# Optimization experiments

Measured on AMD Instinct MI355X. Metric: run time of the kernel, lower is better.

The kernel has to match this reference:

```python
import jax, jax.numpy as jnp
import numpy as np

B, S, DIM = 2, 2048, 4096
N_HEADS, N_KV_HEADS = 32, 8
HEAD_DIM = DIM // N_HEADS  # 128
N_REP = N_HEADS // N_KV_HEADS  # 4
NEG_INF = -1e9


def setup_inputs() -> dict:
    key = jax.random.key(0)
    ks = jax.random.split(key, 6)
    x = jax.random.normal(ks[0], (B, S, DIM), dtype=jnp.float32)
    # torch Linear weights are [out_features, in_features]
    sc = 0.02
    wq = jax.random.normal(ks[1], (N_HEADS * HEAD_DIM, DIM), dtype=jnp.float32) * sc
    wk = jax.random.normal(ks[2], (N_KV_HEADS * HEAD_DIM, DIM), dtype=jnp.float32) * sc
    wv = jax.random.normal(ks[3], (N_KV_HEADS * HEAD_DIM, DIM), dtype=jnp.float32) * sc
    wo = jax.random.normal(ks[4], (DIM, N_HEADS * HEAD_DIM), dtype=jnp.float32) * sc
    # RoPE frequencies, matching llama precompute_freqs_cis (theta=10000)
    inv = 1.0 / (10000.0 ** (np.arange(0, HEAD_DIM, 2, dtype=np.float32) / HEAD_DIM))
    t = np.arange(S, dtype=np.float32)
    freqs = np.outer(t, inv)  # [S, HEAD_DIM//2]
    freqs_cos = jnp.asarray(np.cos(freqs), dtype=jnp.float32)
    freqs_sin = jnp.asarray(np.sin(freqs), dtype=jnp.float32)
    # causal mask: 0 on/below diagonal, large negative above
    mask = jnp.triu(jnp.full((S, S), NEG_INF, dtype=jnp.float32), k=1)
    return {"x": x, "wq": wq, "wk": wk, "wv": wv, "wo": wo,
            "freqs_cos": freqs_cos, "freqs_sin": freqs_sin,
            "mask": mask, "start_pos": 0}


def _apply_rope(t, cos, sin):
    # t: [b, s, h, hd]; complex mult on interleaved (even, odd) pairs
    tr, ti = t[..., 0::2], t[..., 1::2]
    cos = cos[None, :, None, :]
    sin = sin[None, :, None, :]
    out_r = tr * cos - ti * sin
    out_i = tr * sin + ti * cos
    return jnp.stack([out_r, out_i], axis=-1).reshape(t.shape)


def reference(x, wq, wk, wv, wo, freqs_cos, freqs_sin, mask, start_pos):
    bsz, seqlen, _ = x.shape
    xq = (x @ wq.T).reshape(bsz, seqlen, N_HEADS, HEAD_DIM)
    xk = (x @ wk.T).reshape(bsz, seqlen, N_KV_HEADS, HEAD_DIM)
    xv = (x @ wv.T).reshape(bsz, seqlen, N_KV_HEADS, HEAD_DIM)
    xq = _apply_rope(xq, freqs_cos, freqs_sin)
    xk = _apply_rope(xk, freqs_cos, freqs_sin)
    # prefill: start_pos == 0, so cache slice == current keys/values
    # GQA repeat_kv via broadcast (torch repeat_interleave over head dim)
    keys = jnp.broadcast_to(xk[:, :, :, None, :],
                            (bsz, seqlen, N_KV_HEADS, N_REP, HEAD_DIM)
                            ).reshape(bsz, seqlen, N_HEADS, HEAD_DIM)
    values = jnp.broadcast_to(xv[:, :, :, None, :],
                              (bsz, seqlen, N_KV_HEADS, N_REP, HEAD_DIM)
                              ).reshape(bsz, seqlen, N_HEADS, HEAD_DIM)
    scale = 1.0 / jnp.sqrt(jnp.float32(HEAD_DIM))
    # [b, h, q, k]
    scores = jnp.einsum('bqhd,bkhd->bhqk', xq, keys) * scale
    scores = scores + mask[None, None, :, :]
    probs = jax.nn.softmax(scores.astype(jnp.float32), axis=-1).astype(xq.dtype)
    out = jnp.einsum('bhqk,bkhd->bqhd', probs, values)
    out = out.reshape(bsz, seqlen, N_HEADS * HEAD_DIM)
    return out @ wo.T
```

## Files before the change

### kernel.cpp

```cpp
#include <hip/hip_runtime.h>

typedef unsigned short u16;
typedef unsigned int u32;
typedef __bf16 bf16_t;
typedef bf16_t bf16x8 __attribute__((ext_vector_type(8)));
typedef float f32x4 __attribute__((ext_vector_type(4)));

#define B_ 2
#define S_ 2048
#define DIM_ 4096
#define NH_ 32
#define NKV_ 8
#define HD_ 128

__device__ __forceinline__ u16 f2b(float f) {
  union { float f; unsigned u; } x; x.f = f;
  unsigned r = x.u + 0x7fffu + ((x.u >> 16) & 1u);
  return (u16)(r >> 16);
}
__device__ __forceinline__ float b2f(u16 u) {
  union { unsigned u; float f; } x; x.u = ((unsigned)u) << 16;
  return x.f;
}
__device__ __forceinline__ u32 cvtpk(float lo, float hi) {
  u32 r;
  asm volatile("v_cvt_pk_bf16_f32 %0, %1, %2" : "=v"(r) : "v"(lo), "v"(hi));
  return r;
}

#define GLDS(gsrc, ldst) \
  __builtin_amdgcn_global_load_lds((const __attribute__((address_space(1))) void*)(gsrc), \
                                   (__attribute__((address_space(3))) void*)(ldst), 16, 0, 0)
#define BAR()    __builtin_amdgcn_s_barrier()
#define SCHED0() __builtin_amdgcn_sched_barrier(0)

__global__ void cvt_kernel(const float* __restrict__ in, u16* __restrict__ out, int n4) {
  int i = blockIdx.x * blockDim.x + threadIdx.x;
  int stride = gridDim.x * blockDim.x;
  for (; i < n4; i += stride) {
    float4 v = ((const float4*)in)[i];
    ushort4 o;
    o.x = f2b(v.x); o.y = f2b(v.y); o.z = f2b(v.z); o.w = f2b(v.w);
    ((ushort4*)out)[i] = o;
  }
}

__global__ void rope_kernel(u16* __restrict__ t, const float* __restrict__ fc,
                            const float* __restrict__ fs, int nheads) {
  int idx = blockIdx.x * blockDim.x + threadIdx.x;
  int ppr = nheads * 64;
  int row = idx / ppr;
  int pr = idx - row * ppr;
  int h = pr >> 6, j = pr & 63;
  int s = row & (S_ - 1);
  float c = fc[s * 64 + j], sn = fs[s * 64 + j];
  u16* p = t + (size_t)row * (size_t)(nheads * HD_) + h * HD_ + j * 2;
  float tr = b2f(p[0]), ti = b2f(p[1]);
  p[0] = f2b(tr * c - ti * sn);
  p[1] = f2b(tr * sn + ti * c);
}

template<int MODE>
__global__ __launch_bounds__(512, 2) void gemm256(const u16* __restrict__ A,
                                                  const u16* __restrict__ B,
                                                  void* __restrict__ Cout,
                                                  void* __restrict__ Cout2,
                                                  void* __restrict__ Cout3,
                                                  int M, int N, int K) {
  __shared__ u16 As[2][2][128 * 64];
  __shared__ u16 Bs[2][2][128 * 64];
  const int nbn = N >> 8;
  const int nwg = gridDim.x;
  int wg = blockIdx.x;
  wg = (wg & 7) * (nwg >> 3) + (wg >> 3);
  const int bm = wg / nbn;
  const int bn = wg - bm * nbn;
  const int tid = threadIdx.x;
  const int lane = tid & 63;
  const int wv = tid >> 6;
  const int wm = wv >> 2, wn = wv & 3;
  const int qloc = lane & 15, grp = lane >> 4;
  const int NT = K >> 6;

  f32x4 acc[8][4];
#pragma unroll
  for (int i = 0; i < 8; i++)
#pragma unroll
    for (int j = 0; j < 4; j++)
#pragma unroll
      for (int r = 0; r < 4; r++) acc[i][j][r] = 0.0f;

  const int srowl = lane >> 3;
  const int scsw = 8 * ((lane & 7) ^ srowl);
  const size_t rowA = (size_t)(bm * 256 + wv * 16 + srowl) * K + scsw;
  const size_t rowB = (size_t)(bn * 256 + wv * 16 + srowl) * K + scsw;

#define STAGE_A(buf, h, tt) { \
    GLDS(A + rowA + (size_t)((h) * 128) * K + (size_t)(tt) * 64, &As[buf][h][wv * 1024]); \
    GLDS(A + rowA + (size_t)((h) * 128 + 8) * K + (size_t)(tt) * 64, &As[buf][h][wv * 1024 + 512]); }
#define STAGE_B(buf, h, tt) { \
    GLDS(B + rowB + (size_t)((h) * 128) * K + (size_t)(tt) * 64, &Bs[buf][h][wv * 1024]); \
    GLDS(B + rowB + (size_t)((h) * 128 + 8) * K + (size_t)(tt) * 64, &Bs[buf][h][wv * 1024 + 512]); }

  STAGE_A(0, 0, 0); STAGE_A(0, 1, 0);
  STAGE_B(0, 0, 0); STAGE_B(0, 1, 0);
  STAGE_B(1, 0, 1); STAGE_B(1, 1, 1);
  asm volatile("s_waitcnt vmcnt(4)" ::: "memory");
  BAR();

  for (int t = 0; t < NT; t += 2) {
#pragma unroll
    for (int half = 0; half < 2; half++) {
      bf16x8 bfr[4][2];
#pragma unroll
      for (int qd = 0; qd < 4; qd++) {
        if (qd == 0) {
#pragma unroll
          for (int j = 0; j < 4; j++)
#pragma unroll
            for (int ks = 0; ks < 2; ks++) {
              int rb = (wn & 1) * 64 + j * 16 + qloc;
              bfr[j][ks] = *(const bf16x8*)((const char*)&Bs[half][wn >> 1][0]
                           + rb * 128 + ((ks * 64 + grp * 16) ^ ((rb & 7) << 4)));
            }
        }
        bf16x8 af[2][2];
#pragma unroll
        for (int ii = 0; ii < 2; ii++)
#pragma unroll
          for (int ks = 0; ks < 2; ks++) {
            int rh = qd * 32 + ii * 16 + qloc;
            af[ii][ks] = *(const bf16x8*)((const char*)&As[half][wm][0]
                         + rh * 128 + ((ks * 64 + grp * 16) ^ ((rh & 7) << 4)));
          }
        const int ph = half * 4 + qd;
        if (ph == 0)      { STAGE_A(1, 0, t + 1); }
        else if (ph == 1) { STAGE_A(1, 1, t + 1); }
        else if (ph == 2) { if (t + 2 < NT) STAGE_B(0, 0, t + 2); }
        else if (ph == 3) { if (t + 2 < NT) STAGE_B(0, 1, t + 2); }
        else if (ph == 4) { if (t + 2 < NT) STAGE_A(0, 0, t + 2); }
        else if (ph == 5) { if (t + 2 < NT) STAGE_A(0, 1, t + 2); }
        else if (ph == 6) { if (t + 3 < NT) STAGE_B(1, 0, t + 3); }
        else              { if (t + 3 < NT) STAGE_B(1, 1, t + 3); }
        BAR();
        __builtin_amdgcn_s_setprio(1);
#pragma unroll
        for (int ii = 0; ii < 2; ii++)
#pragma unroll
          for (int ks = 0; ks < 2; ks++)
#pragma unroll
            for (int j = 0; j < 4; j++)
              acc[qd * 2 + ii][j] = __builtin_amdgcn_mfma_f32_16x16x32_bf16(
                  af[ii][ks], bfr[j][ks], acc[qd * 2 + ii][j], 0, 0, 0);
        __builtin_amdgcn_s_setprio(0);
        SCHED0();
        if (qd == 3) {
          if ((half == 0 ? t + 2 : t + 3) < NT)
            asm volatile("s_waitcnt vmcnt(4)" ::: "memory");
          else
            asm volatile("s_waitcnt vmcnt(0)" ::: "memory");
        }
        BAR();
      }
    }
  }
#undef STAGE_A
#undef STAGE_B

  const int r0g = bm * 256 + wm * 128 + grp * 4;
  const int c0g = bn * 256 + wn * 64 + qloc;
#pragma unroll
  for (int i = 0; i < 8; i++)
#pragma unroll
    for (int j = 0; j < 4; j++)
#pragma unroll
      for (int r = 0; r < 4; r++) {
        int row = r0g + i * 16 + r;
        int col = c0g + j * 16;
        float v = acc[i][j][r];
        if (MODE == 1) ((float*)Cout)[(size_t)row * N + col] = v;
        else {
          if (col < 4096)      ((u16*)Cout)[(size_t)row * 4096 + col] = f2b(v);
          else if (col < 5120) ((u16*)Cout2)[(size_t)row * 1024 + (col - 4096)] = f2b(v);
          else                 ((u16*)Cout3)[(size_t)(col - 5120) * M + row] = f2b(v);
        }
      }
}

__global__ __launch_bounds__(256) void attn_kernel(const u16* __restrict__ Q,
                                                   const u16* __restrict__ Kt,
                                                   const u16* __restrict__ VT,
                                                   u16* __restrict__ O,
                                                   const float* __restrict__ fc,
                                                   const float* __restrict__ fs) {
  __shared__ u16 Ks[2][32 * 128];
  __shared__ u16 Vs[2][32 * 128];

  const int bid = blockIdx.x;
  const int qb = 31 - (bid >> 6);
  const int h = bid & 31;
  const int b = (bid >> 5) & 1;
  const int g = h >> 2;
  const int tid = threadIdx.x;
  const int lane = tid & 63;
  const int wv = tid >> 6;
  const int qrow0 = qb * 64 + wv * 16;
  const float scl2 = 0.12751744f;

  const int qloc = lane & 15;
  const int grp = lane >> 4;

  bf16x8 qf[4];
  {
    const int qr = qrow0 + qloc;
    const u16* qptr = Q + (size_t)(b * S_ + qr) * (NH_ * HD_) + h * HD_ + grp * 8;
#pragma unroll
    for (int c = 0; c < 4; c++) {
      union { bf16x8 v; u16 u[8]; } raw;
      raw.v = *(const bf16x8*)(qptr + c * 32);
      const int p0 = c * 16 + grp * 4;
      const float4 cv = *(const float4*)&fc[(size_t)qr * 64 + p0];
      const float4 sv = *(const float4*)&fs[(size_t)qr * 64 + p0];
      union { bf16x8 v; u32 w[4]; } out;
      const float cc[4] = {cv.x, cv.y, cv.z, cv.w};
      const float ss[4] = {sv.x, sv.y, sv.z, sv.w};
#pragma unroll
      for (int j = 0; j < 4; j++) {
        float tr = b2f(raw.u[2 * j]), ti = b2f(raw.u[2 * j + 1]);
        out.w[j] = cvtpk(tr * cc[j] - ti * ss[j], tr * ss[j] + ti * cc[j]);
      }
      qf[c] = out.v;
    }
  }

  float m = -1e30f, l = 0.f;
  f32x4 o[8];
#pragma unroll
  for (int c = 0; c < 8; c++)
#pragma unroll
    for (int r = 0; r < 4; r++) o[c][r] = 0.f;

  const int nkv = 2 * qb + 2;

  const int kkey_ = wv * 4 + grp;
  const int kcb_ = qloc * 16;
  const int vd_ = wv * 16 + (lane >> 2);
  const int vkb_ = (lane & 3) * 16;

  auto STAGE = [&](int t, int buf) {
#pragma unroll
    for (int p = 0; p < 2; p++) {
      int key = p * 16 + kkey_;
      int cbs = kcb_ ^ ((key & 7) << 4);
      const u16* ksrc = Kt + (size_t)(b * S_ + t * 32 + key) * (NKV_ * HD_) + g * HD_ + (cbs >> 1);
      GLDS(ksrc, &Ks[buf][(p * 4 + wv) * 512]);
      int d = p * 64 + vd_;
      int kbs = vkb_ ^ (((d >> 1) & 3) << 4);
      const u16* vsrc = VT + (size_t)(g * HD_ + d) * (B_ * S_) + b * S_ + t * 32 + (kbs >> 1);
      GLDS(vsrc, &Vs[buf][(p * 4 + wv) * 512]);
    }
  };

  STAGE(0, 0);
  int cur = 0;

  for (int t = 0; t < nkv; t++) {
    const bool pf = (t + 1 < nkv);
    if (pf) {
      STAGE(t + 1, cur ^ 1);
      asm volatile("s_waitcnt vmcnt(4)" ::: "memory");
    } else {
      asm volatile("s_waitcnt vmcnt(0)" ::: "memory");
    }
    BAR();
    SCHED0();

    if (t * 32 <= qrow0 + 15) {
      f32x4 s[2];
      __builtin_amdgcn_s_setprio(1);
#pragma unroll
      for (int n = 0; n < 2; n++) {
        f32x4 sc;
#pragma unroll
        for (int r = 0; r < 4; r++) sc[r] = 0.f;
        int krow = n * 16 + qloc;
#pragma unroll
        for (int c = 0; c < 4; c++) {
          int colb = c * 64 + (grp * 16);
          int addr = krow * 256 + (colb ^ ((krow & 7) << 4));
          bf16x8 kf = *(const bf16x8*)((const char*)Ks[cur] + addr);
          sc = __builtin_amdgcn_mfma_f32_16x16x32_bf16(kf, qf[c], sc, 0, 0, 0);
        }
        s[n] = sc;
      }
      __builtin_amdgcn_s_setprio(0);
      const int q = qrow0 + qloc;
      if (t * 32 + 31 > qrow0) {
#pragma unroll
        for (int n = 0; n < 2; n++)
#pragma unroll
          for (int r = 0; r < 4; r++) {
            int k = t * 32 + n * 16 + grp * 4 + r;
            if (k > q) s[n][r] = -1e9f;
          }
      }
      float pmax = fmaxf(fmaxf(fmaxf(s[0][0], s[0][1]), fmaxf(s[0][2], s[0][3])),
                         fmaxf(fmaxf(s[1][0], s[1][1]), fmaxf(s[1][2], s[1][3])));
      pmax = fmaxf(pmax, __shfl_xor(pmax, 16));
      pmax = fmaxf(pmax, __shfl_xor(pmax, 32));
      if (__any(pmax > m + 64.f)) {
        float mn = fmaxf(m, pmax);
        float alpha = exp2f((m - mn) * scl2);
        m = mn;
        l *= alpha;
        float ar[4];
#pragma unroll
        for (int r = 0; r < 4; r++) ar[r] = __shfl(alpha, grp * 4 + r);
#pragma unroll
        for (int c = 0; c < 8; c++)
#pragma unroll
          for (int r = 0; r < 4; r++) o[c][r] *= ar[r];
      }
      const float msc = m * scl2;
      float p[2][4];
#pragma unroll
      for (int n = 0; n < 2; n++)
#pragma unroll
        for (int r = 0; r < 4; r++)
          p[n][r] = exp2f(fmaf(s[n][r], scl2, -msc));
      float rs = ((p[0][0] + p[0][1]) + (p[0][2] + p[0][3])) +
                 ((p[1][0] + p[1][1]) + (p[1][2] + p[1][3]));
      rs += __shfl_xor(rs, 16);
      rs += __shfl_xor(rs, 32);
      l += rs;
      u32 a0 = cvtpk(p[0][0], p[0][1]);
      u32 a1 = cvtpk(p[0][2], p[0][3]);
      u32 b0 = cvtpk(p[1][0], p[1][1]);
      u32 b1 = cvtpk(p[1][2], p[1][3]);
      asm volatile("v_permlane32_swap_b32 %0, %1" : "+v"(a0), "+v"(b0));
      asm volatile("v_permlane32_swap_b32 %0, %1" : "+v"(a1), "+v"(b1));
      asm volatile("v_permlane16_swap_b32 %0, %1" : "+v"(a0), "+v"(b0));
      asm volatile("v_permlane16_swap_b32 %0, %1" : "+v"(a1), "+v"(b1));
      union { bf16x8 v; u32 w[4]; } pau;
      pau.w[0] = a0; pau.w[1] = a1; pau.w[2] = b0; pau.w[3] = b1;
      bf16x8 pa = pau.v;
      __builtin_amdgcn_s_setprio(1);
#pragma unroll
      for (int c = 0; c < 8; c++) {
        int d = c * 16 + qloc;
        int addr = d * 64 + ((grp * 16) ^ (((d >> 1) & 3) << 4));
        bf16x8 vf = *(const bf16x8*)((const char*)Vs[cur] + addr);
        o[c] = __builtin_amdgcn_mfma_f32_16x16x32_bf16(pa, vf, o[c], 0, 0, 0);
      }
      __builtin_amdgcn_s_setprio(0);
    }
    asm volatile("s_waitcnt lgkmcnt(0)" ::: "memory");
    SCHED0();
    BAR();
    cur ^= 1;
  }

  float lr[4];
#pragma unroll
  for (int r = 0; r < 4; r++) lr[r] = 1.0f / __shfl(l, grp * 4 + r);
#pragma unroll
  for (int c = 0; c < 8; c++)
#pragma unroll
    for (int r = 0; r < 4; r++) {
      int qo = qrow0 + grp * 4 + r;
      float val = o[c][r] * lr[r];
      O[(size_t)(b * S_ + qo) * (NH_ * HD_) + h * HD_ + c * 16 + qloc] = f2b(val);
    }
}

extern "C" void kernel_launch(void* const* d_in, const int* in_sizes, int n_in,
                              void* d_out, int out_size, void* d_ws, size_t ws_size,
                              hipStream_t stream) {
  const float* x  = (const float*)d_in[0];
  const float* wq = (const float*)d_in[1];
  const float* wk = (const float*)d_in[2];
  const float* wv = (const float*)d_in[3];
  const float* wo = (const float*)d_in[4];
  const float* fc = (const float*)d_in[5];
  const float* fs = (const float*)d_in[6];

  char* ws = (char*)d_ws;
  u16* Xb   = (u16*)(ws);
  u16* Wqkv = (u16*)(ws + 33554432);
  u16* Qw   = (u16*)(ws + 83886080);
  u16* Kw   = (u16*)(ws + 117440512);
  u16* Vw   = (u16*)(ws + 125829120);
  u16* Ow   = Xb;
  u16* Wob  = Wqkv;

  auto cvt = [&](const float* in, u16* out, int n) {
    int n4 = n >> 2;
    int blocks = (n4 + 255) / 256; if (blocks > 2048) blocks = 2048;
    cvt_kernel<<<dim3(blocks), dim3(256), 0, stream>>>(in, out, n4);
  };
  cvt(x,  Xb,  B_ * S_ * DIM_);
  cvt(wq, Wqkv, DIM_ * DIM_);
  cvt(wk, Wqkv + (size_t)4096 * 4096, NKV_ * HD_ * DIM_);
  cvt(wv, Wqkv + (size_t)5120 * 4096, NKV_ * HD_ * DIM_);

  gemm256<4><<<dim3(16 * 24), 512, 0, stream>>>(Xb, Wqkv, Qw, Kw, Vw, 4096, 6144, 4096);

  cvt(wo, Wob, DIM_ * DIM_);

  rope_kernel<<<dim3((B_ * S_ * NKV_ * 64) / 256), 256, 0, stream>>>(Kw, fc, fs, NKV_);

  attn_kernel<<<dim3(B_ * NH_ * (S_ / 64)), 256, 0, stream>>>(Qw, Kw, Vw, Ow, fc, fs);

  gemm256<1><<<dim3(16 * 16), 512, 0, stream>>>(Ow, Wob, d_out, nullptr, nullptr, 4096, 4096, 4096);
}
```

Measured before the change: 568.0 us.

## Split fused QKV GEMM into Q GEMM and a 128-row-tile KV GEMM

```diff
diff --git a/kernel.cpp b/kernel.cpp
--- a/kernel.cpp
+++ b/kernel.cpp
@@ -60,15 +60,18 @@
   p[1] = f2b(tr * sn + ti * c);
 }
 
-template<int MODE>
+template<int MODE, bool SM>
 __global__ __launch_bounds__(512, 2) void gemm256(const u16* __restrict__ A,
                                                   const u16* __restrict__ B,
                                                   void* __restrict__ Cout,
                                                   void* __restrict__ Cout2,
-                                                  void* __restrict__ Cout3,
                                                   int M, int N, int K) {
-  __shared__ u16 As[2][2][128 * 64];
-  __shared__ u16 Bs[2][2][128 * 64];
+  constexpr int BM = SM ? 128 : 256;
+  constexpr int AH = SM ? 4096 : 8192;
+  constexpr int II = SM ? 1 : 2;
+  constexpr int NACC = SM ? 4 : 8;
+  __shared__ u16 As[2][2][AH];
+  __shared__ u16 Bs[2][2][8192];
   const int nbn = N >> 8;
   const int nwg = gridDim.x;
   int wg = blockIdx.x;
@@ -82,9 +85,9 @@
   const int qloc = lane & 15, grp = lane >> 4;
   const int NT = K >> 6;
 
-  f32x4 acc[8][4];
-#pragma unroll
-  for (int i = 0; i < 8; i++)
+  f32x4 acc[NACC][4];
+#pragma unroll
+  for (int i = 0; i < NACC; i++)
 #pragma unroll
     for (int j = 0; j < 4; j++)
 #pragma unroll
@@ -92,12 +95,16 @@
 
   const int srowl = lane >> 3;
   const int scsw = 8 * ((lane & 7) ^ srowl);
-  const size_t rowA = (size_t)(bm * 256 + wv * 16 + srowl) * K + scsw;
+  const size_t rowA = SM ? ((size_t)(bm * 128 + wv * 8 + srowl) * K + scsw)
+                         : ((size_t)(bm * 256 + wv * 16 + srowl) * K + scsw);
   const size_t rowB = (size_t)(bn * 256 + wv * 16 + srowl) * K + scsw;
 
 #define STAGE_A(buf, h, tt) { \
-    GLDS(A + rowA + (size_t)((h) * 128) * K + (size_t)(tt) * 64, &As[buf][h][wv * 1024]); \
-    GLDS(A + rowA + (size_t)((h) * 128 + 8) * K + (size_t)(tt) * 64, &As[buf][h][wv * 1024 + 512]); }
+    if (SM) { \
+      GLDS(A + rowA + (size_t)((h) * 64) * K + (size_t)(tt) * 64, &As[buf][h][wv * 512]); \
+    } else { \
+      GLDS(A + rowA + (size_t)((h) * 128) * K + (size_t)(tt) * 64, &As[buf][h][wv * 1024]); \
+      GLDS(A + rowA + (size_t)((h) * 128 + 8) * K + (size_t)(tt) * 64, &As[buf][h][wv * 1024 + 512]); } }
 #define STAGE_B(buf, h, tt) { \
     GLDS(B + rowB + (size_t)((h) * 128) * K + (size_t)(tt) * 64, &Bs[buf][h][wv * 1024]); \
     GLDS(B + rowB + (size_t)((h) * 128 + 8) * K + (size_t)(tt) * 64, &Bs[buf][h][wv * 1024 + 512]); }
@@ -124,12 +131,12 @@
                            + rb * 128 + ((ks * 64 + grp * 16) ^ ((rb & 7) << 4)));
             }
         }
-        bf16x8 af[2][2];
-#pragma unroll
-        for (int ii = 0; ii < 2; ii++)
+        bf16x8 af[II][2];
+#pragma unroll
+        for (int ii = 0; ii < II; ii++)
 #pragma unroll
           for (int ks = 0; ks < 2; ks++) {
-            int rh = qd * 32 + ii * 16 + qloc;
+            int rh = SM ? (qd * 16 + qloc) : (qd * 32 + ii * 16 + qloc);
             af[ii][ks] = *(const bf16x8*)((const char*)&As[half][wm][0]
                          + rh * 128 + ((ks * 64 + grp * 16) ^ ((rh & 7) << 4)));
           }
@@ -145,13 +152,13 @@
         BAR();
         __builtin_amdgcn_s_setprio(1);
 #pragma unroll
-        for (int ii = 0; ii < 2; ii++)
+        for (int ii = 0; ii < II; ii++)
 #pragma unroll
           for (int ks = 0; ks < 2; ks++)
 #pragma unroll
             for (int j = 0; j < 4; j++)
-              acc[qd * 2 + ii][j] = __builtin_amdgcn_mfma_f32_16x16x32_bf16(
-                  af[ii][ks], bfr[j][ks], acc[qd * 2 + ii][j], 0, 0, 0);
+              acc[qd * II + ii][j] = __builtin_amdgcn_mfma_f32_16x16x32_bf16(
+                  af[ii][ks], bfr[j][ks], acc[qd * II + ii][j], 0, 0, 0);
         __builtin_amdgcn_s_setprio(0);
         SCHED0();
         if (qd == 3) {
@@ -167,10 +174,10 @@
 #undef STAGE_A
 #undef STAGE_B
 
-  const int r0g = bm * 256 + wm * 128 + grp * 4;
+  const int r0g = bm * BM + wm * (BM / 2) + grp * 4;
   const int c0g = bn * 256 + wn * 64 + qloc;
 #pragma unroll
-  for (int i = 0; i < 8; i++)
+  for (int i = 0; i < NACC; i++)
 #pragma unroll
     for (int j = 0; j < 4; j++)
 #pragma unroll
@@ -178,11 +185,11 @@
         int row = r0g + i * 16 + r;
         int col = c0g + j * 16;
         float v = acc[i][j][r];
-        if (MODE == 1) ((float*)Cout)[(size_t)row * N + col] = v;
+        if (MODE == 1)      ((float*)Cout)[(size_t)row * N + col] = v;
+        else if (MODE == 0) ((u16*)Cout)[(size_t)row * N + col]  = f2b(v);
         else {
-          if (col < 4096)      ((u16*)Cout)[(size_t)row * 4096 + col] = f2b(v);
-          else if (col < 5120) ((u16*)Cout2)[(size_t)row * 1024 + (col - 4096)] = f2b(v);
-          else                 ((u16*)Cout3)[(size_t)(col - 5120) * M + row] = f2b(v);
+          if (col < 1024) ((u16*)Cout)[(size_t)row * 1024 + col] = f2b(v);
+          else            ((u16*)Cout2)[(size_t)(col - 1024) * M + row] = f2b(v);
         }
       }
 }
@@ -385,13 +392,14 @@
   const float* fs = (const float*)d_in[6];
 
   char* ws = (char*)d_ws;
-  u16* Xb   = (u16*)(ws);
-  u16* Wqkv = (u16*)(ws + 33554432);
-  u16* Qw   = (u16*)(ws + 83886080);
-  u16* Kw   = (u16*)(ws + 117440512);
-  u16* Vw   = (u16*)(ws + 125829120);
-  u16* Ow   = Xb;
-  u16* Wob  = Wqkv;
+  u16* Xb  = (u16*)(ws);
+  u16* Wqb = (u16*)(ws + 33554432);
+  u16* Wkv = (u16*)(ws + 67108864);
+  u16* Qw  = (u16*)(ws + 83886080);
+  u16* Kw  = (u16*)(ws + 117440512);
+  u16* Vw  = (u16*)(ws + 125829120);
+  u16* Ow  = Xb;
+  u16* Wob = Wqb;
 
   auto cvt = [&](const float* in, u16* out, int n) {
     int n4 = n >> 2;
@@ -399,11 +407,12 @@
     cvt_kernel<<<dim3(blocks), dim3(256), 0, stream>>>(in, out, n4);
   };
   cvt(x,  Xb,  B_ * S_ * DIM_);
-  cvt(wq, Wqkv, DIM_ * DIM_);
-  cvt(wk, Wqkv + (size_t)4096 * 4096, NKV_ * HD_ * DIM_);
-  cvt(wv, Wqkv + (size_t)5120 * 4096, NKV_ * HD_ * DIM_);
-
-  gemm256<4><<<dim3(16 * 24), 512, 0, stream>>>(Xb, Wqkv, Qw, Kw, Vw, 4096, 6144, 4096);
+  cvt(wq, Wqb, DIM_ * DIM_);
+  cvt(wk, Wkv, NKV_ * HD_ * DIM_);
+  cvt(wv, Wkv + (size_t)1024 * 4096, NKV_ * HD_ * DIM_);
+
+  gemm256<0, false><<<dim3(16 * 16), 512, 0, stream>>>(Xb, Wqb, Qw, nullptr, 4096, 4096, 4096);
+  gemm256<3, true><<<dim3(32 * 8), 512, 0, stream>>>(Xb, Wkv, Kw, Vw, 4096, 2048, 4096);
 
   cvt(wo, Wob, DIM_ * DIM_);
 
@@ -411,5 +420,5 @@
 
   attn_kernel<<<dim3(B_ * NH_ * (S_ / 64)), 256, 0, stream>>>(Qw, Kw, Vw, Ow, fc, fs);
 
-  gemm256<1><<<dim3(16 * 16), 512, 0, stream>>>(Ow, Wob, d_out, nullptr, nullptr, 4096, 4096, 4096);
-}
+  gemm256<1, false><<<dim3(16 * 16), 512, 0, stream>>>(Ow, Wob, d_out, nullptr, 4096, 4096, 4096);
+}
```

Measured after the change: 536.6 us. 1.06x faster.
